# Kernel optimization log

Measured on AMD Instinct MI355X. Metric: run time of the kernel, lower is better.

## Reference

```python
import jax, jax.numpy as jnp
import numpy as np

N_NODES = 100000
IN_CH = 2
HID = 64
K = 3
N_EDGES = 1600000


def _cheb_norm(edge_index, num_nodes):
    # PyG ChebConv sym normalization with lambda_max=2.0:
    # L_hat = L - I = -D^{-1/2} A D^{-1/2} (zero diagonal, edge_weight=1)
    src, dst = edge_index[0], edge_index[1]
    deg = jax.ops.segment_sum(jnp.ones(src.shape[0], jnp.float32), src,
                              num_segments=num_nodes)
    dinv = jnp.where(deg > 0, jax.lax.rsqrt(jnp.maximum(deg, 1.0)), 0.0)
    norm = -dinv[src] * dinv[dst]  # [E]
    return src, dst, norm


def _cheb_conv(x, src, dst, norm, W, b, num_nodes):
    # W: [K, in, out], b: [out]
    def prop(t):  # sparse L_hat @ t via gather/scatter
        return jax.ops.segment_sum(norm[:, None] * t[src], dst,
                                   num_segments=num_nodes)
    Tx0 = x
    out = Tx0 @ W[0]
    Tx1 = prop(Tx0)
    out = out + Tx1 @ W[1]
    for k in range(2, W.shape[0]):
        Tx2 = 2.0 * prop(Tx1) - Tx0
        out = out + Tx2 @ W[k]
        Tx0, Tx1 = Tx1, Tx2
    return out + b


def setup_inputs() -> dict:
    key = jax.random.key(0)
    ks = jax.random.split(key, 16)
    x = jax.random.normal(ks[0], (N_NODES, IN_CH), jnp.float32)
    edge_index = jax.random.randint(ks[1], (2, N_EDGES), 0, N_NODES,
                                    dtype=jnp.int64)
    h = jax.random.normal(ks[2], (N_NODES, HID), jnp.float32)
    s1 = 1.0 / np.sqrt(IN_CH)
    s2 = 1.0 / np.sqrt(HID)
    sg = 1.0 / np.sqrt(2 * HID)
    W1 = jax.random.uniform(ks[3], (K, IN_CH, HID), jnp.float32, -s1, s1)
    b1 = jnp.zeros((HID,), jnp.float32)
    W2 = jax.random.uniform(ks[4], (K, HID, HID), jnp.float32, -s2, s2)
    b2 = jnp.zeros((HID,), jnp.float32)
    Wz = jax.random.uniform(ks[5], (2 * HID, HID), jnp.float32, -sg, sg)
    bz = jax.random.uniform(ks[6], (HID,), jnp.float32, -sg, sg)
    Wr = jax.random.uniform(ks[7], (2 * HID, HID), jnp.float32, -sg, sg)
    br = jax.random.uniform(ks[8], (HID,), jnp.float32, -sg, sg)
    Wc = jax.random.uniform(ks[9], (2 * HID, HID), jnp.float32, -sg, sg)
    bc = jax.random.uniform(ks[10], (HID,), jnp.float32, -sg, sg)
    return {"x": x, "edge_index": edge_index, "h": h,
            "W1": W1, "b1": b1, "W2": W2, "b2": b2,
            "Wz": Wz, "bz": bz, "Wr": Wr, "br": br, "Wc": Wc, "bc": bc}


def reference(x, edge_index, h, W1, b1, W2, b2, Wz, bz, Wr, br, Wc, bc):
    num_nodes = x.shape[0]
    src, dst, norm = _cheb_norm(edge_index, num_nodes)
    input_conv = _cheb_conv(x, src, dst, norm, W1, b1, num_nodes)
    hidden_conv = _cheb_conv(h, src, dst, norm, W2, b2, num_nodes)
    combined = jnp.concatenate([input_conv, hidden_conv], axis=1)
    z = jax.nn.sigmoid(combined @ Wz + bz)
    r = jax.nn.sigmoid(combined @ Wr + br)
    comb_c = jnp.concatenate([input_conv, r * hidden_conv], axis=1)
    h_tilde = jnp.tanh(comb_c @ Wc + bc)
    return z * h + (1.0 - z) * h_tilde
```

## Files before the change

kernel.cpp:

```cpp
#include <hip/hip_runtime.h>
#include <hip/hip_bf16.h>
#include <math.h>

#define HID 64
#define NBA 512
#define NBUCK 256
#define BSHIFT 9
#define BINS 512
#define NBN (NBUCK * NBA)

typedef __attribute__((ext_vector_type(8))) short bf16x8;
typedef __attribute__((ext_vector_type(4))) float f32x4;

__device__ __forceinline__ unsigned int bf16r(float f) {
    unsigned int u = __float_as_uint(f);
    return (u + 0x7fffu + ((u >> 16) & 1u)) >> 16;
}
__device__ __forceinline__ unsigned int pack2(float a, float b) {
    return bf16r(a) | (bf16r(b) << 16);
}
__device__ __forceinline__ float lo2f(unsigned int u) { return __uint_as_float(u << 16); }
__device__ __forceinline__ float hi2f(unsigned int u) { return __uint_as_float(u & 0xffff0000u); }

__device__ __forceinline__ bf16x8 asbf(uint4 u) {
    union { uint4 u4; bf16x8 b; } c; c.u4 = u; return c.b;
}
__device__ __forceinline__ void load8(const float* p, float* d) {
    float4 a = *(const float4*)p, b = *(const float4*)(p + 4);
    d[0]=a.x; d[1]=a.y; d[2]=a.z; d[3]=a.w; d[4]=b.x; d[5]=b.y; d[6]=b.z; d[7]=b.w;
}

__global__ void bucketA_kernel(const int* __restrict__ ei, int E,
                               int* __restrict__ cntsc) {
    __shared__ int cd[NBUCK], cs[NBUCK];
    int t = threadIdx.x;
    cd[t] = 0; cs[t] = 0;
    __syncthreads();
    int ce = (E + NBA - 1) / NBA;
    int e0 = blockIdx.x * ce, e1 = min(e0 + ce, E);
    for (int e = e0 + t; e < e1; e += 256) {
        int s = ei[e], d = ei[E + e];
        atomicAdd(&cs[s >> BSHIFT], 1);
        atomicAdd(&cd[d >> BSHIFT], 1);
    }
    __syncthreads();
    cntsc[t * NBA + blockIdx.x]       = cd[t];
    cntsc[NBN + t * NBA + blockIdx.x] = cs[t];
}

__global__ void scanA_kernel(const int* __restrict__ cnt, int* __restrict__ bs, int N) {
    __shared__ int s[256];
    int t = threadIdx.x, n = blockIdx.x * 256 + t;
    s[t] = (n < N) ? cnt[n] : 0;
    __syncthreads();
    for (int off = 128; off > 0; off >>= 1) {
        if (t < off) s[t] += s[t + off];
        __syncthreads();
    }
    if (t == 0) bs[blockIdx.x] = s[0];
}

__global__ void scanB_kernel(int* __restrict__ bs, int nb) {
    __shared__ int s[1024];
    int t = threadIdx.x;
    int orig = (t < nb) ? bs[t] : 0;
    s[t] = orig;
    __syncthreads();
    for (int off = 1; off < 1024; off <<= 1) {
        int v = (t >= off) ? s[t - off] : 0;
        __syncthreads();
        s[t] += v;
        __syncthreads();
    }
    if (t < nb) bs[t] = s[t] - orig;
}

__global__ void scanC_kernel(const int* __restrict__ cnt, const int* __restrict__ bs,
                             int* __restrict__ outp, int N) {
    __shared__ int s[256];
    int t = threadIdx.x, n = blockIdx.x * 256 + t;
    int c = (n < N) ? cnt[n] : 0;
    s[t] = c;
    __syncthreads();
    for (int off = 1; off < 256; off <<= 1) {
        int v = (t >= off) ? s[t - off] : 0;
        __syncthreads();
        s[t] += v;
        __syncthreads();
    }
    if (n < N) outp[n] = bs[blockIdx.x] + s[t] - c;
}

__global__ void bucketB_kernel(const int* __restrict__ ei, int E,
                               const int* __restrict__ scanned,
                               int2* __restrict__ dstrec, int* __restrict__ srckeys) {
    __shared__ int cd[NBUCK], cs[NBUCK], bd[NBUCK], bsr[NBUCK];
    int t = threadIdx.x;
    cd[t] = 0; cs[t] = 0;
    bd[t]  = scanned[t * NBA + blockIdx.x];
    bsr[t] = scanned[NBN + t * NBA + blockIdx.x] - E;
    __syncthreads();
    int ce = (E + NBA - 1) / NBA;
    int e0 = blockIdx.x * ce, e1 = min(e0 + ce, E);
    for (int e = e0 + t; e < e1; e += 256) {
        int s = ei[e], d = ei[E + e];
        int db = d >> BSHIFT, sb = s >> BSHIFT;
        int rd = atomicAdd(&cd[db], 1);
        dstrec[bd[db] + rd] = make_int2(d, s);
        int rs = atomicAdd(&cs[sb], 1);
        srckeys[bsr[sb] + rs] = s;
    }
}

__global__ void bucketC2_kernel(const int* __restrict__ srckeys,
                                const int* __restrict__ scanned,
                                float* __restrict__ dinv, int N, int E) {
    __shared__ int deg[BINS];
    int b = blockIdx.x, t = threadIdx.x;
    deg[t] = 0;
    __syncthreads();
    int start = scanned[NBN + b * NBA] - E;
    int end   = (b < NBUCK - 1) ? scanned[NBN + (b + 1) * NBA] - E : E;
    for (int i = start + t; i < end; i += BINS)
        atomicAdd(&deg[srckeys[i] & (BINS - 1)], 1);
    __syncthreads();
    int node = (b << BSHIFT) + t;
    if (node < N) {
        int dg = deg[t];
        dinv[node] = dg > 0 ? rsqrtf((float)dg) : 0.0f;
    }
}

__global__ void bucketC1_kernel(const int2* __restrict__ dstrec,
                                const int* __restrict__ scanned,
                                const float* __restrict__ dinv,
                                int* __restrict__ row, int* __restrict__ cnt,
                                int2* __restrict__ srcw, int N, int E) {
    __shared__ int lc[BINS], ls[BINS], lr[BINS];
    int b = blockIdx.x, t = threadIdx.x;
    lc[t] = 0; lr[t] = 0;
    __syncthreads();
    int start = scanned[b * NBA];
    int end   = (b < NBUCK - 1) ? scanned[(b + 1) * NBA] : E;
    for (int i = start + t; i < end; i += BINS)
        atomicAdd(&lc[dstrec[i].x & (BINS - 1)], 1);
    __syncthreads();
    ls[t] = lc[t];
    __syncthreads();
    for (int off = 1; off < BINS; off <<= 1) {
        int v = (t >= off) ? ls[t - off] : 0;
        __syncthreads();
        ls[t] += v;
        __syncthreads();
    }
    int rl = start + ls[t] - lc[t];
    int node = (b << BSHIFT) + t;
    if (node < N) { row[node] = rl; cnt[node] = lc[t]; }
    __syncthreads();
    ls[t] = rl;
    __syncthreads();
    for (int i = start + t; i < end; i += BINS) {
        int2 rec = dstrec[i];
        int bin = rec.x & (BINS - 1);
        int p = ls[bin] + atomicAdd(&lr[bin], 1);
        srcw[p] = make_int2(rec.y, __float_as_int(dinv[rec.y]));
    }
}

__global__ void packwT_kernel(const float* __restrict__ W2, const float* __restrict__ Wz,
                              const float* __restrict__ Wr, const float* __restrict__ Wc,
                              unsigned int* __restrict__ WT) {
    int idx = blockIdx.x * blockDim.x + threadIdx.x;
    if (idx >= 18432) return;
    float v0, v1;
    if (idx < 6144) {
        int c = idx / 96, kk = idx % 96;
        int k0 = 2 * kk;
        if (k0 < 64) {
            v0 = W2[k0 * 64 + c] - W2[8192 + k0 * 64 + c];
            v1 = W2[(k0 + 1) * 64 + c] - W2[8192 + (k0 + 1) * 64 + c];
        } else if (k0 < 128) {
            v0 = W2[4096 + (k0 - 64) * 64 + c];
            v1 = W2[4096 + (k0 - 63) * 64 + c];
        } else {
            v0 = 2.0f * W2[8192 + (k0 - 128) * 64 + c];
            v1 = 2.0f * W2[8192 + (k0 - 127) * 64 + c];
        }
    } else if (idx < 14336) {
        int t = idx - 6144;
        int c = t / 64, kk = t % 64, k0 = 2 * kk;
        const float* Ws = (c < 64) ? Wz : Wr;
        int cc = c & 63;
        v0 = Ws[k0 * 64 + cc];
        v1 = Ws[(k0 + 1) * 64 + cc];
    } else {
        int t = idx - 14336;
        int c = t / 64, kk = t % 64, k0 = 2 * kk;
        v0 = Wc[k0 * 64 + c];
        v1 = Wc[(k0 + 1) * 64 + c];
    }
    WT[idx] = pack2(v0, v1);
}

__global__ void packh_kernel(const float* __restrict__ h, unsigned int* __restrict__ hbf,
                             int total2) {
    int i = blockIdx.x * blockDim.x + threadIdx.x;
    if (i < total2) {
        float2 v = ((const float2*)h)[i];
        hbf[i] = pack2(v.x, v.y);
    }
}

__global__ void gather2_kernel(const int* __restrict__ row, const int* __restrict__ cnt,
                               const int2* __restrict__ srcw, const float* __restrict__ dinv,
                               const float* __restrict__ xsrc, float* __restrict__ dst, int N) {
    int tid = threadIdx.x;
    int n = blockIdx.x * 16 + (tid >> 4);
    if (n >= N) return;
    int t = tid & 15;
    int start = row[n], k = cnt[n];
    float a0 = 0.0f, a1 = 0.0f;
    const float2* x2 = (const float2*)xsrc;
    for (int e = t; e < k; e += 16) {
        int2 rec = srcw[start + e];
        float w = __int_as_float(rec.y);
        float2 xv = x2[rec.x];
        a0 = fmaf(w, xv.x, a0);
        a1 = fmaf(w, xv.y, a1);
    }
    a0 += __shfl_xor(a0, 1); a1 += __shfl_xor(a1, 1);
    a0 += __shfl_xor(a0, 2); a1 += __shfl_xor(a1, 2);
    a0 += __shfl_xor(a0, 4); a1 += __shfl_xor(a1, 4);
    a0 += __shfl_xor(a0, 8); a1 += __shfl_xor(a1, 8);
    if (t == 0) {
        float dn = -dinv[n];
        ((float2*)dst)[n] = make_float2(dn * a0, dn * a1);
    }
}

__global__ void gather64_kernel(const int* __restrict__ row, const int* __restrict__ cnt,
                                const int2* __restrict__ srcw, const float* __restrict__ dinv,
                                const unsigned int* __restrict__ src,
                                unsigned int* __restrict__ dst, int N) {
    int wu = __builtin_amdgcn_readfirstlane((int)threadIdx.x >> 6);
    int n = blockIdx.x * 4 + wu;
    if (n >= N) return;
    int lane = threadIdx.x & 63;
    int t    = lane & 7;
    int slot = lane >> 3;
    int start = row[n], k = cnt[n];
    float a0 = 0, a1 = 0, a2 = 0, a3 = 0, a4 = 0, a5 = 0, a6 = 0, a7 = 0;
    for (int e = slot; e < k; e += 16) {
        int2 rec0 = srcw[start + e];
        bool h2 = (e + 8) < k;
        int2 rec1 = h2 ? srcw[start + e + 8] : rec0;
        uint4 v0 = ((const uint4*)(src + (size_t)rec0.x * 32))[t];
        uint4 v1 = ((const uint4*)(src + (size_t)rec1.x * 32))[t];
        float w0 = __int_as_float(rec0.y);
        float w1 = h2 ? __int_as_float(rec1.y) : 0.0f;
        a0 = fmaf(w0, lo2f(v0.x), a0); a1 = fmaf(w0, hi2f(v0.x), a1);
        a2 = fmaf(w0, lo2f(v0.y), a2); a3 = fmaf(w0, hi2f(v0.y), a3);
        a4 = fmaf(w0, lo2f(v0.z), a4); a5 = fmaf(w0, hi2f(v0.z), a5);
        a6 = fmaf(w0, lo2f(v0.w), a6); a7 = fmaf(w0, hi2f(v0.w), a7);
        a0 = fmaf(w1, lo2f(v1.x), a0); a1 = fmaf(w1, hi2f(v1.x), a1);
        a2 = fmaf(w1, lo2f(v1.y), a2); a3 = fmaf(w1, hi2f(v1.y), a3);
        a4 = fmaf(w1, lo2f(v1.z), a4); a5 = fmaf(w1, hi2f(v1.z), a5);
        a6 = fmaf(w1, lo2f(v1.w), a6); a7 = fmaf(w1, hi2f(v1.w), a7);
    }
    a0 += __shfl_xor(a0, 8);  a1 += __shfl_xor(a1, 8);
    a2 += __shfl_xor(a2, 8);  a3 += __shfl_xor(a3, 8);
    a4 += __shfl_xor(a4, 8);  a5 += __shfl_xor(a5, 8);
    a6 += __shfl_xor(a6, 8);  a7 += __shfl_xor(a7, 8);
    a0 += __shfl_xor(a0, 16); a1 += __shfl_xor(a1, 16);
    a2 += __shfl_xor(a2, 16); a3 += __shfl_xor(a3, 16);
    a4 += __shfl_xor(a4, 16); a5 += __shfl_xor(a5, 16);
    a6 += __shfl_xor(a6, 16); a7 += __shfl_xor(a7, 16);
    a0 += __shfl_xor(a0, 32); a1 += __shfl_xor(a1, 32);
    a2 += __shfl_xor(a2, 32); a3 += __shfl_xor(a3, 32);
    a4 += __shfl_xor(a4, 32); a5 += __shfl_xor(a5, 32);
    a6 += __shfl_xor(a6, 32); a7 += __shfl_xor(a7, 32);
    if (slot == 0) {
        float dn = -dinv[n];
        uint4 o;
        o.x = pack2(dn * a0, dn * a1);
        o.y = pack2(dn * a2, dn * a3);
        o.z = pack2(dn * a4, dn * a5);
        o.w = pack2(dn * a6, dn * a7);
        ((uint4*)(dst + (size_t)n * 32))[t] = o;
    }
}

__global__ __launch_bounds__(256, 2) void gate_mfma_kernel(
    float* __restrict__ out,
    const float* __restrict__ x,
    const float* __restrict__ h,
    const float* __restrict__ txa,
    const float* __restrict__ txb,
    const unsigned int* __restrict__ t1u,
    const unsigned int* __restrict__ ppu,
    const float* __restrict__ W1, const float* __restrict__ b1,
    const unsigned int* __restrict__ WT,
    const float* __restrict__ b2, const float* __restrict__ bz,
    const float* __restrict__ br, const float* __restrict__ bc,
    int N) {
    __shared__ __align__(16) unsigned int s_wzr[128 * 68];
    __shared__ __align__(16) unsigned int s_wc [64 * 68];
    __shared__ unsigned short tr[4][32][72];

    int tid  = threadIdx.x;
    int lane = tid & 63;
    int wu   = __builtin_amdgcn_readfirstlane(tid >> 6);
    int q    = lane >> 4;
    int r16  = lane & 15;
    int base = blockIdx.x * 128 + wu * 32;

    int nA[2];
    nA[0] = min(base + r16, N - 1);
    nA[1] = min(base + 16 + r16, N - 1);

    const unsigned int* W2eT = WT;

    {
        const uint4* wzr4 = (const uint4*)(WT + 6144);
        const uint4* wc4  = (const uint4*)(WT + 14336);
        #pragma unroll
        for (int i = 0; i < 8; ++i) {
            int idx4 = tid + i * 256;
            uint4 v = wzr4[idx4];
            int r = idx4 >> 4, c4 = (idx4 & 15) * 4;
            *(uint4*)&s_wzr[r * 68 + c4] = v;
        }
        #pragma unroll
        for (int i = 0; i < 4; ++i) {
            int idx4 = tid + i * 256;
            uint4 v = wc4[idx4];
            int r = idx4 >> 4, c4 = (idx4 & 15) * 4;
            *(uint4*)&s_wc[r * 68 + c4] = v;
        }
    }

    uint4 icA[2][2];
    {
        float2 xv[2], tav[2], tbv[2];
        #pragma unroll
        for (int mt = 0; mt < 2; ++mt) {
            xv[mt]  = ((const float2*)x)[nA[mt]];
            tav[mt] = ((const float2*)txa)[nA[mt]];
            tbv[mt] = ((const float2*)txb)[nA[mt]];
        }
        #pragma unroll
        for (int kf = 0; kf < 2; ++kf) {
            int ch0 = kf * 32 + 8 * q;
            float b1s[8], w0[8], w1s[8], w2[8], w3[8], w4[8], w5[8];
            load8(b1 + ch0, b1s);
            load8(W1 + ch0, w0);       load8(W1 + 64 + ch0, w1s);
            load8(W1 + 128 + ch0, w2); load8(W1 + 192 + ch0, w3);
            load8(W1 + 256 + ch0, w4); load8(W1 + 320 + ch0, w5);
            #pragma unroll
            for (int mt = 0; mt < 2; ++mt) {
                float t20 = 2.0f * tbv[mt].x - xv[mt].x;
                float t21 = 2.0f * tbv[mt].y - xv[mt].y;
                unsigned int pr[4];
                #pragma unroll
                for (int p = 0; p < 4; ++p) {
                    float v0 = b1s[2*p]   + xv[mt].x * w0[2*p]   + xv[mt].y * w1s[2*p]
                             + tav[mt].x * w2[2*p]   + tav[mt].y * w3[2*p]
                             + t20 * w4[2*p]   + t21 * w5[2*p];
                    float v1 = b1s[2*p+1] + xv[mt].x * w0[2*p+1] + xv[mt].y * w1s[2*p+1]
                             + tav[mt].x * w2[2*p+1] + tav[mt].y * w3[2*p+1]
                             + t20 * w4[2*p+1] + t21 * w5[2*p+1];
                    pr[p] = pack2(v0, v1);
                }
                icA[mt][kf] = make_uint4(pr[0], pr[1], pr[2], pr[3]);
            }
        }
    }

    f32x4 acc1[2][4];
    #pragma unroll
    for (int mt = 0; mt < 2; ++mt)
        #pragma unroll
        for (int nt = 0; nt < 4; ++nt)
            acc1[mt][nt] = (f32x4){0.0f, 0.0f, 0.0f, 0.0f};

    #pragma unroll
    for (int ks = 0; ks < 6; ++ks) {
        bf16x8 a[2];
        if (ks < 2) {
            #pragma unroll
            for (int mt = 0; mt < 2; ++mt) {
                float hs[8];
                load8(h + (size_t)nA[mt] * 64 + ks * 32 + 8 * q, hs);
                uint4 u;
                u.x = pack2(hs[0], hs[1]); u.y = pack2(hs[2], hs[3]);
                u.z = pack2(hs[4], hs[5]); u.w = pack2(hs[6], hs[7]);
                a[mt] = asbf(u);
            }
        } else {
            const unsigned int* tab = (ks < 4) ? t1u : ppu;
            int ksl = ks & 1;
            #pragma unroll
            for (int mt = 0; mt < 2; ++mt)
                a[mt] = asbf(*(const uint4*)(tab + (size_t)nA[mt] * 32 + ksl * 16 + q * 4));
        }
        #pragma unroll
        for (int nt = 0; nt < 4; ++nt) {
            bf16x8 b = asbf(*(const uint4*)(W2eT + (nt * 16 + r16) * 96 + ks * 16 + q * 4));
            #pragma unroll
            for (int mt = 0; mt < 2; ++mt)
                acc1[mt][nt] = __builtin_amdgcn_mfma_f32_16x16x32_bf16(a[mt], b, acc1[mt][nt], 0, 0, 0);
        }
    }

    __syncthreads();

    float b2v[4];
    #pragma unroll
    for (int nt = 0; nt < 4; ++nt) b2v[nt] = b2[nt * 16 + r16];
    #pragma unroll
    for (int mt = 0; mt < 2; ++mt)
        #pragma unroll
        for (int nt = 0; nt < 4; ++nt)
            #pragma unroll
            for (int reg = 0; reg < 4; ++reg) {
                acc1[mt][nt][reg] += b2v[nt];
                tr[wu][mt * 16 + 4 * q + reg][nt * 16 + r16] =
                    (unsigned short)bf16r(acc1[mt][nt][reg]);
            }
    __builtin_amdgcn_wave_barrier();
    bf16x8 hcA[2][2];
    #pragma unroll
    for (int mt = 0; mt < 2; ++mt)
        #pragma unroll
        for (int kf = 0; kf < 2; ++kf)
            hcA[mt][kf] = asbf(*(const uint4*)&tr[wu][mt * 16 + r16][kf * 32 + 8 * q]);
    __builtin_amdgcn_wave_barrier();

    f32x4 acc2[2][8];
    #pragma unroll
    for (int mt = 0; mt < 2; ++mt)
        #pragma unroll
        for (int nt = 0; nt < 8; ++nt)
            acc2[mt][nt] = (f32x4){0.0f, 0.0f, 0.0f, 0.0f};

    #pragma unroll
    for (int kf = 0; kf < 4; ++kf) {
        bf16x8 a[2];
        a[0] = (kf < 2) ? asbf(icA[0][kf]) : hcA[0][kf - 2];
        a[1] = (kf < 2) ? asbf(icA[1][kf]) : hcA[1][kf - 2];
        #pragma unroll
        for (int nt = 0; nt < 8; ++nt) {
            bf16x8 b = asbf(*(const uint4*)&s_wzr[(nt * 16 + r16) * 68 + kf * 16 + q * 4]);
            #pragma unroll
            for (int mt = 0; mt < 2; ++mt)
                acc2[mt][nt] = __builtin_amdgcn_mfma_f32_16x16x32_bf16(a[mt], b, acc2[mt][nt], 0, 0, 0);
        }
    }

    float bzv[4], brv[4];
    #pragma unroll
    for (int nt = 0; nt < 4; ++nt) { bzv[nt] = bz[nt * 16 + r16]; brv[nt] = br[nt * 16 + r16]; }
    float zz[2][4][4];
    #pragma unroll
    for (int mt = 0; mt < 2; ++mt)
        #pragma unroll
        for (int nt = 0; nt < 4; ++nt)
            #pragma unroll
            for (int reg = 0; reg < 4; ++reg) {
                zz[mt][nt][reg] = 1.0f / (1.0f + __expf(-(acc2[mt][nt][reg] + bzv[nt])));
                float rr = 1.0f / (1.0f + __expf(-(acc2[mt][nt + 4][reg] + brv[nt])));
                float rhc = rr * acc1[mt][nt][reg];
                tr[wu][mt * 16 + 4 * q + reg][nt * 16 + r16] = (unsigned short)bf16r(rhc);
            }
    __builtin_amdgcn_wave_barrier();
    bf16x8 rhcA[2][2];
    #pragma unroll
    for (int mt = 0; mt < 2; ++mt)
        #pragma unroll
        for (int kf = 0; kf < 2; ++kf)
            rhcA[mt][kf] = asbf(*(const uint4*)&tr[wu][mt * 16 + r16][kf * 32 + 8 * q]);
    __builtin_amdgcn_wave_barrier();

    f32x4 acc3[2][4];
    #pragma unroll
    for (int mt = 0; mt < 2; ++mt)
        #pragma unroll
        for (int nt = 0; nt < 4; ++nt)
            acc3[mt][nt] = (f32x4){0.0f, 0.0f, 0.0f, 0.0f};

    #pragma unroll
    for (int kf = 0; kf < 4; ++kf) {
        bf16x8 a[2];
        a[0] = (kf < 2) ? asbf(icA[0][kf]) : rhcA[0][kf - 2];
        a[1] = (kf < 2) ? asbf(icA[1][kf]) : rhcA[1][kf - 2];
        #pragma unroll
        for (int nt = 0; nt < 4; ++nt) {
            bf16x8 b = asbf(*(const uint4*)&s_wc[(nt * 16 + r16) * 68 + kf * 16 + q * 4]);
            #pragma unroll
            for (int mt = 0; mt < 2; ++mt)
                acc3[mt][nt] = __builtin_amdgcn_mfma_f32_16x16x32_bf16(a[mt], b, acc3[mt][nt], 0, 0, 0);
        }
    }

    float bcv[4];
    #pragma unroll
    for (int nt = 0; nt < 4; ++nt) bcv[nt] = bc[nt * 16 + r16];
    #pragma unroll
    for (int mt = 0; mt < 2; ++mt)
        #pragma unroll
        for (int nt = 0; nt < 4; ++nt)
            #pragma unroll
            for (int reg = 0; reg < 4; ++reg) {
                int node = base + mt * 16 + 4 * q + reg;
                if (node < N) {
                    float a = acc3[mt][nt][reg] + bcv[nt];
                    a = fminf(fmaxf(a, -40.0f), 40.0f);
                    float e = __expf(2.0f * a);
                    float ht = 1.0f - 2.0f / (e + 1.0f);
                    float hv = h[(size_t)node * 64 + nt * 16 + r16];
                    float z = zz[mt][nt][reg];
                    out[(size_t)node * 64 + nt * 16 + r16] = z * hv + (1.0f - z) * ht;
                }
            }
}

extern "C" void kernel_launch(void* const* d_in, const int* in_sizes, int n_in,
                              void* d_out, int out_size, void* d_ws, size_t ws_size,
                              hipStream_t stream) {
    const float* x  = (const float*)d_in[0];
    const int*   ei = (const int*)  d_in[1];
    const float* h  = (const float*)d_in[2];
    const float* W1 = (const float*)d_in[3];
    const float* b1 = (const float*)d_in[4];
    const float* W2 = (const float*)d_in[5];
    const float* b2 = (const float*)d_in[6];
    const float* Wz = (const float*)d_in[7];
    const float* bz = (const float*)d_in[8];
    const float* Wr = (const float*)d_in[9];
    const float* br = (const float*)d_in[10];
    const float* Wc = (const float*)d_in[11];
    const float* bc = (const float*)d_in[12];
    float* out = (float*)d_out;

    int N = in_sizes[0] / 2;
    int E = in_sizes[1] / 2;

    char* wsb = (char*)d_ws;
    float* dinv = (float*)wsb;
    int*   row  = (int*)  (wsb + (size_t)N * 4);
    int*   cnt  = (int*)  (wsb + (size_t)2 * N * 4);
    float* txa  = (float*)(wsb + (size_t)3 * N * 4);
    float* txb  = (float*)(wsb + (size_t)5 * N * 4);
    int*   bs   = (int*)  (wsb + (size_t)7 * N * 4);
    unsigned int* WT = (unsigned int*)(wsb + ((size_t)7 * N + 1024) * 4);
    int*   cntsc   = (int*)(wsb + ((size_t)7 * N + 19456) * 4);
    int*   scanned = (int*)(wsb + ((size_t)7 * N + 19456 + 2 * NBN) * 4);
    int2*  srcw = (int2*)(wsb + ((size_t)7 * N + 19456 + 4 * NBN) * 4);
    size_t O = (size_t)7 * N + 19456 + 4 * (size_t)NBN + 2 * (size_t)E;
    unsigned int* bufA = (unsigned int*)(wsb + O * 4);
    unsigned int* hpp  = (unsigned int*)(wsb + (O + (size_t)32 * N) * 4);
    int2*  dstrec  = (int2*)(wsb + O * 4);
    int*   srckeys = (int*) (wsb + (O + 2 * (size_t)E) * 4);

    bucketA_kernel<<<NBA, 256, 0, stream>>>(ei, E, cntsc);
    int scn = 2 * NBN;
    scanA_kernel<<<scn / 256, 256, 0, stream>>>(cntsc, bs, scn);
    scanB_kernel<<<1, 1024, 0, stream>>>(bs, scn / 256);
    scanC_kernel<<<scn / 256, 256, 0, stream>>>(cntsc, bs, scanned, scn);
    bucketB_kernel<<<NBA, 256, 0, stream>>>(ei, E, scanned, dstrec, srckeys);
    bucketC2_kernel<<<NBUCK, BINS, 0, stream>>>(srckeys, scanned, dinv, N, E);
    bucketC1_kernel<<<NBUCK, BINS, 0, stream>>>(dstrec, scanned, dinv, row, cnt, srcw, N, E);

    packwT_kernel<<<(18432 + 255) / 256, 256, 0, stream>>>(W2, Wz, Wr, Wc, WT);
    packh_kernel <<<(32 * N + 255) / 256, 256, 0, stream>>>(h, hpp, 32 * N);

    int g2blocks = (N + 15) / 16;
    gather2_kernel<<<g2blocks, 256, 0, stream>>>(row, cnt, srcw, dinv, x,   txa, N);
    gather2_kernel<<<g2blocks, 256, 0, stream>>>(row, cnt, srcw, dinv, txa, txb, N);

    int gblocks = (N + 3) / 4;
    gather64_kernel<<<gblocks, 256, 0, stream>>>(row, cnt, srcw, dinv, hpp,  bufA, N);
    gather64_kernel<<<gblocks, 256, 0, stream>>>(row, cnt, srcw, dinv, bufA, hpp,  N);

    int gateblocks = (N + 127) / 128;
    gate_mfma_kernel<<<gateblocks, 256, 0, stream>>>(
        out, x, h, txa, txb, bufA, hpp, W1, b1, WT, b2, bz, br, bc, N);
}
```

Baseline: 240.4 us.

## Fuse 2-channel x propagation into 64-channel gather via padded row layout

Each node row of the bf16 h table is padded to 36 words so it also holds the two fp32 x features. The 64-channel gather then propagates both x and h in the same pass, which removes the two separate gather2 launches and their repeated reads of the edge list. Separately, the bucketing record is packed into one 32-bit word (17-bit src plus 9-bit local dst), halving that intermediate's traffic. The costs are a padded 144-byte row stride that is no longer a power of two, so loads may straddle cache lines, and an assumption that node ids fit in 17 bits.

```diff
diff --git a/kernel.cpp b/kernel.cpp
--- a/kernel.cpp
+++ b/kernel.cpp
@@ -8,6 +8,7 @@
 #define BSHIFT 9
 #define BINS 512
 #define NBN (NBUCK * NBA)
+#define RSTRIDE 36
 
 typedef __attribute__((ext_vector_type(8))) short bf16x8;
 typedef __attribute__((ext_vector_type(4))) float f32x4;
@@ -93,7 +94,8 @@
 
 __global__ void bucketB_kernel(const int* __restrict__ ei, int E,
                                const int* __restrict__ scanned,
-                               int2* __restrict__ dstrec, int* __restrict__ srckeys) {
+                               unsigned int* __restrict__ dstrec,
+                               int* __restrict__ srckeys) {
     __shared__ int cd[NBUCK], cs[NBUCK], bd[NBUCK], bsr[NBUCK];
     int t = threadIdx.x;
     cd[t] = 0; cs[t] = 0;
@@ -106,7 +108,7 @@
         int s = ei[e], d = ei[E + e];
         int db = d >> BSHIFT, sb = s >> BSHIFT;
         int rd = atomicAdd(&cd[db], 1);
-        dstrec[bd[db] + rd] = make_int2(d, s);
+        dstrec[bd[db] + rd] = (unsigned int)s | ((unsigned int)(d & (BINS - 1)) << 17);
         int rs = atomicAdd(&cs[sb], 1);
         srckeys[bsr[sb] + rs] = s;
     }
@@ -131,7 +133,7 @@
     }
 }
 
-__global__ void bucketC1_kernel(const int2* __restrict__ dstrec,
+__global__ void bucketC1_kernel(const unsigned int* __restrict__ dstrec,
                                 const int* __restrict__ scanned,
                                 const float* __restrict__ dinv,
                                 int* __restrict__ row, int* __restrict__ cnt,
@@ -143,7 +145,7 @@
     int start = scanned[b * NBA];
     int end   = (b < NBUCK - 1) ? scanned[(b + 1) * NBA] : E;
     for (int i = start + t; i < end; i += BINS)
-        atomicAdd(&lc[dstrec[i].x & (BINS - 1)], 1);
+        atomicAdd(&lc[dstrec[i] >> 17], 1);
     __syncthreads();
     ls[t] = lc[t];
     __syncthreads();
@@ -160,10 +162,11 @@
     ls[t] = rl;
     __syncthreads();
     for (int i = start + t; i < end; i += BINS) {
-        int2 rec = dstrec[i];
-        int bin = rec.x & (BINS - 1);
+        unsigned int rec = dstrec[i];
+        int bin = (int)(rec >> 17);
+        int src = (int)(rec & 0x1FFFFu);
         int p = ls[bin] + atomicAdd(&lr[bin], 1);
-        srcw[p] = make_int2(rec.y, __float_as_int(dinv[rec.y]));
+        srcw[p] = make_int2(src, __float_as_int(dinv[src]));
     }
 }
 
@@ -202,39 +205,17 @@
     WT[idx] = pack2(v0, v1);
 }
 
-__global__ void packh_kernel(const float* __restrict__ h, unsigned int* __restrict__ hbf,
-                             int total2) {
+__global__ void packh_kernel(const float* __restrict__ h, const float* __restrict__ x,
+                             unsigned int* __restrict__ tab, int N) {
     int i = blockIdx.x * blockDim.x + threadIdx.x;
-    if (i < total2) {
-        float2 v = ((const float2*)h)[i];
-        hbf[i] = pack2(v.x, v.y);
-    }
-}
-
-__global__ void gather2_kernel(const int* __restrict__ row, const int* __restrict__ cnt,
-                               const int2* __restrict__ srcw, const float* __restrict__ dinv,
-                               const float* __restrict__ xsrc, float* __restrict__ dst, int N) {
-    int tid = threadIdx.x;
-    int n = blockIdx.x * 16 + (tid >> 4);
-    if (n >= N) return;
-    int t = tid & 15;
-    int start = row[n], k = cnt[n];
-    float a0 = 0.0f, a1 = 0.0f;
-    const float2* x2 = (const float2*)xsrc;
-    for (int e = t; e < k; e += 16) {
-        int2 rec = srcw[start + e];
-        float w = __int_as_float(rec.y);
-        float2 xv = x2[rec.x];
-        a0 = fmaf(w, xv.x, a0);
-        a1 = fmaf(w, xv.y, a1);
-    }
-    a0 += __shfl_xor(a0, 1); a1 += __shfl_xor(a1, 1);
-    a0 += __shfl_xor(a0, 2); a1 += __shfl_xor(a1, 2);
-    a0 += __shfl_xor(a0, 4); a1 += __shfl_xor(a1, 4);
-    a0 += __shfl_xor(a0, 8); a1 += __shfl_xor(a1, 8);
-    if (t == 0) {
-        float dn = -dinv[n];
-        ((float2*)dst)[n] = make_float2(dn * a0, dn * a1);
+    if (i >= 34 * N) return;
+    int n = i / 34, w = i - n * 34;
+    unsigned int* rowp = tab + (size_t)n * RSTRIDE;
+    if (w < 32) {
+        float2 v = ((const float2*)h)[n * 32 + w];
+        rowp[w] = pack2(v.x, v.y);
+    } else {
+        rowp[w] = __float_as_uint(x[2 * n + (w - 32)]);
     }
 }
 
@@ -250,43 +231,56 @@
     int slot = lane >> 3;
     int start = row[n], k = cnt[n];
     float a0 = 0, a1 = 0, a2 = 0, a3 = 0, a4 = 0, a5 = 0, a6 = 0, a7 = 0;
+    float ax0 = 0, ax1 = 0;
     for (int e = slot; e < k; e += 16) {
         int2 rec0 = srcw[start + e];
         bool h2 = (e + 8) < k;
         int2 rec1 = h2 ? srcw[start + e + 8] : rec0;
-        uint4 v0 = ((const uint4*)(src + (size_t)rec0.x * 32))[t];
-        uint4 v1 = ((const uint4*)(src + (size_t)rec1.x * 32))[t];
+        const unsigned int* r0 = src + (size_t)rec0.x * RSTRIDE;
+        const unsigned int* r1 = src + (size_t)rec1.x * RSTRIDE;
+        uint4 v0 = ((const uint4*)r0)[t];
+        uint4 v1 = ((const uint4*)r1)[t];
+        float2 xv0 = *(const float2*)(r0 + 32);
+        float2 xv1 = *(const float2*)(r1 + 32);
         float w0 = __int_as_float(rec0.y);
         float w1 = h2 ? __int_as_float(rec1.y) : 0.0f;
         a0 = fmaf(w0, lo2f(v0.x), a0); a1 = fmaf(w0, hi2f(v0.x), a1);
         a2 = fmaf(w0, lo2f(v0.y), a2); a3 = fmaf(w0, hi2f(v0.y), a3);
         a4 = fmaf(w0, lo2f(v0.z), a4); a5 = fmaf(w0, hi2f(v0.z), a5);
         a6 = fmaf(w0, lo2f(v0.w), a6); a7 = fmaf(w0, hi2f(v0.w), a7);
+        ax0 = fmaf(w0, xv0.x, ax0);    ax1 = fmaf(w0, xv0.y, ax1);
         a0 = fmaf(w1, lo2f(v1.x), a0); a1 = fmaf(w1, hi2f(v1.x), a1);
         a2 = fmaf(w1, lo2f(v1.y), a2); a3 = fmaf(w1, hi2f(v1.y), a3);
         a4 = fmaf(w1, lo2f(v1.z), a4); a5 = fmaf(w1, hi2f(v1.z), a5);
         a6 = fmaf(w1, lo2f(v1.w), a6); a7 = fmaf(w1, hi2f(v1.w), a7);
+        ax0 = fmaf(w1, xv1.x, ax0);    ax1 = fmaf(w1, xv1.y, ax1);
     }
     a0 += __shfl_xor(a0, 8);  a1 += __shfl_xor(a1, 8);
     a2 += __shfl_xor(a2, 8);  a3 += __shfl_xor(a3, 8);
     a4 += __shfl_xor(a4, 8);  a5 += __shfl_xor(a5, 8);
     a6 += __shfl_xor(a6, 8);  a7 += __shfl_xor(a7, 8);
+    ax0 += __shfl_xor(ax0, 8);  ax1 += __shfl_xor(ax1, 8);
     a0 += __shfl_xor(a0, 16); a1 += __shfl_xor(a1, 16);
     a2 += __shfl_xor(a2, 16); a3 += __shfl_xor(a3, 16);
     a4 += __shfl_xor(a4, 16); a5 += __shfl_xor(a5, 16);
     a6 += __shfl_xor(a6, 16); a7 += __shfl_xor(a7, 16);
+    ax0 += __shfl_xor(ax0, 16); ax1 += __shfl_xor(ax1, 16);
     a0 += __shfl_xor(a0, 32); a1 += __shfl_xor(a1, 32);
     a2 += __shfl_xor(a2, 32); a3 += __shfl_xor(a3, 32);
     a4 += __shfl_xor(a4, 32); a5 += __shfl_xor(a5, 32);
     a6 += __shfl_xor(a6, 32); a7 += __shfl_xor(a7, 32);
+    ax0 += __shfl_xor(ax0, 32); ax1 += __shfl_xor(ax1, 32);
     if (slot == 0) {
         float dn = -dinv[n];
+        unsigned int* drow = dst + (size_t)n * RSTRIDE;
         uint4 o;
         o.x = pack2(dn * a0, dn * a1);
         o.y = pack2(dn * a2, dn * a3);
         o.z = pack2(dn * a4, dn * a5);
         o.w = pack2(dn * a6, dn * a7);
-        ((uint4*)(dst + (size_t)n * 32))[t] = o;
+        ((uint4*)drow)[t] = o;
+        if (t == 0)
+            *(float2*)(drow + 32) = make_float2(dn * ax0, dn * ax1);
     }
 }
 
@@ -294,8 +288,6 @@
     float* __restrict__ out,
     const float* __restrict__ x,
     const float* __restrict__ h,
-    const float* __restrict__ txa,
-    const float* __restrict__ txb,
     const unsigned int* __restrict__ t1u,
     const unsigned int* __restrict__ ppu,
     const float* __restrict__ W1, const float* __restrict__ b1,
@@ -345,8 +337,8 @@
         #pragma unroll
         for (int mt = 0; mt < 2; ++mt) {
             xv[mt]  = ((const float2*)x)[nA[mt]];
-            tav[mt] = ((const float2*)txa)[nA[mt]];
-            tbv[mt] = ((const float2*)txb)[nA[mt]];
+            tav[mt] = *(const float2*)(t1u + (size_t)nA[mt] * RSTRIDE + 32);
+            tbv[mt] = *(const float2*)(ppu + (size_t)nA[mt] * RSTRIDE + 32);
         }
         #pragma unroll
         for (int kf = 0; kf < 2; ++kf) {
@@ -401,7 +393,7 @@
             int ksl = ks & 1;
             #pragma unroll
             for (int mt = 0; mt < 2; ++mt)
-                a[mt] = asbf(*(const uint4*)(tab + (size_t)nA[mt] * 32 + ksl * 16 + q * 4));
+                a[mt] = asbf(*(const uint4*)(tab + (size_t)nA[mt] * RSTRIDE + ksl * 16 + q * 4));
         }
         #pragma unroll
         for (int nt = 0; nt < 4; ++nt) {
@@ -549,18 +541,16 @@
     float* dinv = (float*)wsb;
     int*   row  = (int*)  (wsb + (size_t)N * 4);
     int*   cnt  = (int*)  (wsb + (size_t)2 * N * 4);
-    float* txa  = (float*)(wsb + (size_t)3 * N * 4);
-    float* txb  = (float*)(wsb + (size_t)5 * N * 4);
-    int*   bs   = (int*)  (wsb + (size_t)7 * N * 4);
-    unsigned int* WT = (unsigned int*)(wsb + ((size_t)7 * N + 1024) * 4);
-    int*   cntsc   = (int*)(wsb + ((size_t)7 * N + 19456) * 4);
-    int*   scanned = (int*)(wsb + ((size_t)7 * N + 19456 + 2 * NBN) * 4);
-    int2*  srcw = (int2*)(wsb + ((size_t)7 * N + 19456 + 4 * NBN) * 4);
-    size_t O = (size_t)7 * N + 19456 + 4 * (size_t)NBN + 2 * (size_t)E;
+    int*   bs   = (int*)  (wsb + (size_t)3 * N * 4);
+    unsigned int* WT = (unsigned int*)(wsb + ((size_t)3 * N + 1024) * 4);
+    int*   cntsc   = (int*)(wsb + ((size_t)3 * N + 19456) * 4);
+    int*   scanned = (int*)(wsb + ((size_t)3 * N + 19456 + 2 * NBN) * 4);
+    int2*  srcw = (int2*)(wsb + ((size_t)3 * N + 19456 + 4 * NBN) * 4);
+    size_t O = (size_t)3 * N + 19456 + 4 * (size_t)NBN + 2 * (size_t)E;
     unsigned int* bufA = (unsigned int*)(wsb + O * 4);
-    unsigned int* hpp  = (unsigned int*)(wsb + (O + (size_t)32 * N) * 4);
-    int2*  dstrec  = (int2*)(wsb + O * 4);
-    int*   srckeys = (int*) (wsb + (O + 2 * (size_t)E) * 4);
+    unsigned int* hpp  = (unsigned int*)(wsb + (O + (size_t)36 * N) * 4);
+    unsigned int* dstrec = (unsigned int*)(wsb + O * 4);
+    int* srckeys = (int*)(wsb + (O + (size_t)E) * 4);
 
     bucketA_kernel<<<NBA, 256, 0, stream>>>(ei, E, cntsc);
     int scn = 2 * NBN;
@@ -572,11 +562,7 @@
     bucketC1_kernel<<<NBUCK, BINS, 0, stream>>>(dstrec, scanned, dinv, row, cnt, srcw, N, E);
 
     packwT_kernel<<<(18432 + 255) / 256, 256, 0, stream>>>(W2, Wz, Wr, Wc, WT);
-    packh_kernel <<<(32 * N + 255) / 256, 256, 0, stream>>>(h, hpp, 32 * N);
-
-    int g2blocks = (N + 15) / 16;
-    gather2_kernel<<<g2blocks, 256, 0, stream>>>(row, cnt, srcw, dinv, x,   txa, N);
-    gather2_kernel<<<g2blocks, 256, 0, stream>>>(row, cnt, srcw, dinv, txa, txb, N);
+    packh_kernel <<<(34 * N + 255) / 256, 256, 0, stream>>>(h, x, hpp, N);
 
     int gblocks = (N + 3) / 4;
     gather64_kernel<<<gblocks, 256, 0, stream>>>(row, cnt, srcw, dinv, hpp,  bufA, N);
@@ -584,5 +570,5 @@
 
     int gateblocks = (N + 127) / 128;
     gate_mfma_kernel<<<gateblocks, 256, 0, stream>>>(
-        out, x, h, txa, txb, bufA, hpp, W1, b1, WT, b2, bz, br, bc, N);
-}
+        out, x, h, bufA, hpp, W1, b1, WT, b2, bz, br, bc, N);
+}
```

Measured after the change: 233.3 us, median of 2. -3.0%, faster.

## Fuse 2-channel gathers into 64-channel gather and compact bucket records

Applied to the files above, without the earlier changes.

Removes the separate gather2 kernels and folds propagation of the 2-channel input into the 64-channel gather, so each edge record and source index is loaded once for both signals. The gather loop is unrolled to four edges per slot, with a one-shot path for nodes of degree at most 16. Destination bucket records are packed into one 32-bit word (17-bit source plus 9-bit bin) instead of int2, which halves that scratch traffic. The packing assumes node ids fit in 17 bits, and the extra accumulators add register pressure.

```diff
diff --git a/kernel.cpp b/kernel.cpp
--- a/kernel.cpp
+++ b/kernel.cpp
@@ -93,7 +93,8 @@
 
 __global__ void bucketB_kernel(const int* __restrict__ ei, int E,
                                const int* __restrict__ scanned,
-                               int2* __restrict__ dstrec, int* __restrict__ srckeys) {
+                               unsigned int* __restrict__ dstrec,
+                               int* __restrict__ srckeys) {
     __shared__ int cd[NBUCK], cs[NBUCK], bd[NBUCK], bsr[NBUCK];
     int t = threadIdx.x;
     cd[t] = 0; cs[t] = 0;
@@ -106,7 +107,7 @@
         int s = ei[e], d = ei[E + e];
         int db = d >> BSHIFT, sb = s >> BSHIFT;
         int rd = atomicAdd(&cd[db], 1);
-        dstrec[bd[db] + rd] = make_int2(d, s);
+        dstrec[bd[db] + rd] = (unsigned int)s | ((unsigned int)(d & (BINS - 1)) << 17);
         int rs = atomicAdd(&cs[sb], 1);
         srckeys[bsr[sb] + rs] = s;
     }
@@ -131,7 +132,7 @@
     }
 }
 
-__global__ void bucketC1_kernel(const int2* __restrict__ dstrec,
+__global__ void bucketC1_kernel(const unsigned int* __restrict__ dstrec,
                                 const int* __restrict__ scanned,
                                 const float* __restrict__ dinv,
                                 int* __restrict__ row, int* __restrict__ cnt,
@@ -143,7 +144,7 @@
     int start = scanned[b * NBA];
     int end   = (b < NBUCK - 1) ? scanned[(b + 1) * NBA] : E;
     for (int i = start + t; i < end; i += BINS)
-        atomicAdd(&lc[dstrec[i].x & (BINS - 1)], 1);
+        atomicAdd(&lc[dstrec[i] >> 17], 1);
     __syncthreads();
     ls[t] = lc[t];
     __syncthreads();
@@ -160,10 +161,11 @@
     ls[t] = rl;
     __syncthreads();
     for (int i = start + t; i < end; i += BINS) {
-        int2 rec = dstrec[i];
-        int bin = rec.x & (BINS - 1);
+        unsigned int rec = dstrec[i];
+        int bin = (int)(rec >> 17);
+        int src = (int)(rec & 0x1FFFFu);
         int p = ls[bin] + atomicAdd(&lr[bin], 1);
-        srcw[p] = make_int2(rec.y, __float_as_int(dinv[rec.y]));
+        srcw[p] = make_int2(src, __float_as_int(dinv[src]));
     }
 }
 
@@ -211,37 +213,19 @@
     }
 }
 
-__global__ void gather2_kernel(const int* __restrict__ row, const int* __restrict__ cnt,
-                               const int2* __restrict__ srcw, const float* __restrict__ dinv,
-                               const float* __restrict__ xsrc, float* __restrict__ dst, int N) {
-    int tid = threadIdx.x;
-    int n = blockIdx.x * 16 + (tid >> 4);
-    if (n >= N) return;
-    int t = tid & 15;
-    int start = row[n], k = cnt[n];
-    float a0 = 0.0f, a1 = 0.0f;
-    const float2* x2 = (const float2*)xsrc;
-    for (int e = t; e < k; e += 16) {
-        int2 rec = srcw[start + e];
-        float w = __int_as_float(rec.y);
-        float2 xv = x2[rec.x];
-        a0 = fmaf(w, xv.x, a0);
-        a1 = fmaf(w, xv.y, a1);
-    }
-    a0 += __shfl_xor(a0, 1); a1 += __shfl_xor(a1, 1);
-    a0 += __shfl_xor(a0, 2); a1 += __shfl_xor(a1, 2);
-    a0 += __shfl_xor(a0, 4); a1 += __shfl_xor(a1, 4);
-    a0 += __shfl_xor(a0, 8); a1 += __shfl_xor(a1, 8);
-    if (t == 0) {
-        float dn = -dinv[n];
-        ((float2*)dst)[n] = make_float2(dn * a0, dn * a1);
-    }
-}
+#define FMA8(ww, vv, xvv) \
+    a0 = fmaf(ww, lo2f(vv.x), a0); a1 = fmaf(ww, hi2f(vv.x), a1); \
+    a2 = fmaf(ww, lo2f(vv.y), a2); a3 = fmaf(ww, hi2f(vv.y), a3); \
+    a4 = fmaf(ww, lo2f(vv.z), a4); a5 = fmaf(ww, hi2f(vv.z), a5); \
+    a6 = fmaf(ww, lo2f(vv.w), a6); a7 = fmaf(ww, hi2f(vv.w), a7); \
+    ax0 = fmaf(ww, xvv.x, ax0);    ax1 = fmaf(ww, xvv.y, ax1);
 
 __global__ void gather64_kernel(const int* __restrict__ row, const int* __restrict__ cnt,
                                 const int2* __restrict__ srcw, const float* __restrict__ dinv,
                                 const unsigned int* __restrict__ src,
-                                unsigned int* __restrict__ dst, int N) {
+                                const float2* __restrict__ xsrc,
+                                unsigned int* __restrict__ dst,
+                                float2* __restrict__ xdst, int N) {
     int wu = __builtin_amdgcn_readfirstlane((int)threadIdx.x >> 6);
     int n = blockIdx.x * 4 + wu;
     if (n >= N) return;
@@ -250,43 +234,72 @@
     int slot = lane >> 3;
     int start = row[n], k = cnt[n];
     float a0 = 0, a1 = 0, a2 = 0, a3 = 0, a4 = 0, a5 = 0, a6 = 0, a7 = 0;
-    for (int e = slot; e < k; e += 16) {
-        int2 rec0 = srcw[start + e];
-        bool h2 = (e + 8) < k;
-        int2 rec1 = h2 ? srcw[start + e + 8] : rec0;
-        uint4 v0 = ((const uint4*)(src + (size_t)rec0.x * 32))[t];
-        uint4 v1 = ((const uint4*)(src + (size_t)rec1.x * 32))[t];
-        float w0 = __int_as_float(rec0.y);
-        float w1 = h2 ? __int_as_float(rec1.y) : 0.0f;
-        a0 = fmaf(w0, lo2f(v0.x), a0); a1 = fmaf(w0, hi2f(v0.x), a1);
-        a2 = fmaf(w0, lo2f(v0.y), a2); a3 = fmaf(w0, hi2f(v0.y), a3);
-        a4 = fmaf(w0, lo2f(v0.z), a4); a5 = fmaf(w0, hi2f(v0.z), a5);
-        a6 = fmaf(w0, lo2f(v0.w), a6); a7 = fmaf(w0, hi2f(v0.w), a7);
-        a0 = fmaf(w1, lo2f(v1.x), a0); a1 = fmaf(w1, hi2f(v1.x), a1);
-        a2 = fmaf(w1, lo2f(v1.y), a2); a3 = fmaf(w1, hi2f(v1.y), a3);
-        a4 = fmaf(w1, lo2f(v1.z), a4); a5 = fmaf(w1, hi2f(v1.z), a5);
-        a6 = fmaf(w1, lo2f(v1.w), a6); a7 = fmaf(w1, hi2f(v1.w), a7);
+    float ax0 = 0, ax1 = 0;
+    if (k <= 16) {
+        if (slot < k) {
+            int2 rec0 = srcw[start + slot];
+            bool h1 = slot + 8 < k;
+            int2 rec1 = h1 ? srcw[start + slot + 8] : rec0;
+            uint4 v0 = ((const uint4*)(src + (size_t)rec0.x * 32))[t];
+            uint4 v1 = ((const uint4*)(src + (size_t)rec1.x * 32))[t];
+            float2 xv0 = xsrc[rec0.x];
+            float2 xv1 = xsrc[rec1.x];
+            float w0 = __int_as_float(rec0.y);
+            float w1 = h1 ? __int_as_float(rec1.y) : 0.0f;
+            FMA8(w0, v0, xv0)
+            FMA8(w1, v1, xv1)
+        }
+    } else {
+        for (int e = slot; e < k; e += 32) {
+            int2 rec0 = srcw[start + e];
+            bool h1 = (e + 8) < k, h2 = (e + 16) < k, h3 = (e + 24) < k;
+            int2 rec1 = h1 ? srcw[start + e + 8]  : rec0;
+            int2 rec2 = h2 ? srcw[start + e + 16] : rec0;
+            int2 rec3 = h3 ? srcw[start + e + 24] : rec0;
+            uint4 v0 = ((const uint4*)(src + (size_t)rec0.x * 32))[t];
+            uint4 v1 = ((const uint4*)(src + (size_t)rec1.x * 32))[t];
+            uint4 v2 = ((const uint4*)(src + (size_t)rec2.x * 32))[t];
+            uint4 v3 = ((const uint4*)(src + (size_t)rec3.x * 32))[t];
+            float2 xv0 = xsrc[rec0.x];
+            float2 xv1 = xsrc[rec1.x];
+            float2 xv2 = xsrc[rec2.x];
+            float2 xv3 = xsrc[rec3.x];
+            float w0 = __int_as_float(rec0.y);
+            float w1 = h1 ? __int_as_float(rec1.y) : 0.0f;
+            float w2 = h2 ? __int_as_float(rec2.y) : 0.0f;
+            float w3 = h3 ? __int_as_float(rec3.y) : 0.0f;
+            FMA8(w0, v0, xv0)
+            FMA8(w1, v1, xv1)
+            FMA8(w2, v2, xv2)
+            FMA8(w3, v3, xv3)
+        }
     }
     a0 += __shfl_xor(a0, 8);  a1 += __shfl_xor(a1, 8);
     a2 += __shfl_xor(a2, 8);  a3 += __shfl_xor(a3, 8);
     a4 += __shfl_xor(a4, 8);  a5 += __shfl_xor(a5, 8);
     a6 += __shfl_xor(a6, 8);  a7 += __shfl_xor(a7, 8);
+    ax0 += __shfl_xor(ax0, 8);  ax1 += __shfl_xor(ax1, 8);
     a0 += __shfl_xor(a0, 16); a1 += __shfl_xor(a1, 16);
     a2 += __shfl_xor(a2, 16); a3 += __shfl_xor(a3, 16);
     a4 += __shfl_xor(a4, 16); a5 += __shfl_xor(a5, 16);
     a6 += __shfl_xor(a6, 16); a7 += __shfl_xor(a7, 16);
+    ax0 += __shfl_xor(ax0, 16); ax1 += __shfl_xor(ax1, 16);
     a0 += __shfl_xor(a0, 32); a1 += __shfl_xor(a1, 32);
     a2 += __shfl_xor(a2, 32); a3 += __shfl_xor(a3, 32);
     a4 += __shfl_xor(a4, 32); a5 += __shfl_xor(a5, 32);
     a6 += __shfl_xor(a6, 32); a7 += __shfl_xor(a7, 32);
+    ax0 += __shfl_xor(ax0, 32); ax1 += __shfl_xor(ax1, 32);
     if (slot == 0) {
         float dn = -dinv[n];
+        unsigned int* drow = dst + (size_t)n * 32;
         uint4 o;
         o.x = pack2(dn * a0, dn * a1);
         o.y = pack2(dn * a2, dn * a3);
         o.z = pack2(dn * a4, dn * a5);
         o.w = pack2(dn * a6, dn * a7);
-        ((uint4*)(dst + (size_t)n * 32))[t] = o;
+        ((uint4*)drow)[t] = o;
+        if (t == 0)
+            xdst[n] = make_float2(dn * ax0, dn * ax1);
     }
 }
 
@@ -559,8 +572,8 @@
     size_t O = (size_t)7 * N + 19456 + 4 * (size_t)NBN + 2 * (size_t)E;
     unsigned int* bufA = (unsigned int*)(wsb + O * 4);
     unsigned int* hpp  = (unsigned int*)(wsb + (O + (size_t)32 * N) * 4);
-    int2*  dstrec  = (int2*)(wsb + O * 4);
-    int*   srckeys = (int*) (wsb + (O + 2 * (size_t)E) * 4);
+    unsigned int* dstrec = (unsigned int*)(wsb + O * 4);
+    int* srckeys = (int*)(wsb + (O + (size_t)E) * 4);
 
     bucketA_kernel<<<NBA, 256, 0, stream>>>(ei, E, cntsc);
     int scn = 2 * NBN;
@@ -574,13 +587,13 @@
     packwT_kernel<<<(18432 + 255) / 256, 256, 0, stream>>>(W2, Wz, Wr, Wc, WT);
     packh_kernel <<<(32 * N + 255) / 256, 256, 0, stream>>>(h, hpp, 32 * N);
 
-    int g2blocks = (N + 15) / 16;
-    gather2_kernel<<<g2blocks, 256, 0, stream>>>(row, cnt, srcw, dinv, x,   txa, N);
-    gather2_kernel<<<g2blocks, 256, 0, stream>>>(row, cnt, srcw, dinv, txa, txb, N);
-
     int gblocks = (N + 3) / 4;
-    gather64_kernel<<<gblocks, 256, 0, stream>>>(row, cnt, srcw, dinv, hpp,  bufA, N);
-    gather64_kernel<<<gblocks, 256, 0, stream>>>(row, cnt, srcw, dinv, bufA, hpp,  N);
+    gather64_kernel<<<gblocks, 256, 0, stream>>>(row, cnt, srcw, dinv, hpp,
+                                                 (const float2*)x, bufA,
+                                                 (float2*)txa, N);
+    gather64_kernel<<<gblocks, 256, 0, stream>>>(row, cnt, srcw, dinv, bufA,
+                                                 (const float2*)txa, hpp,
+                                                 (float2*)txb, N);
 
     int gateblocks = (N + 127) / 128;
     gate_mfma_kernel<<<gateblocks, 256, 0, stream>>>(
```

Result: faster. 215.9 us (-10.2%).
